# Kernel tuning notes

Measured on AMD Instinct MI355X. Metric: run time of the kernel, lower is better.

## Reference

```python
import jax, jax.numpy as jnp
import numpy as np

N = 50000
IN_F = 128
OUT_F = 128
NRELA = 128
E1 = 400000
E2 = 100000
ALPHA = 0.2   # LeakyReLU slope
D = 0.85      # PageRank damping
EPS = 1e-12


def setup_inputs() -> dict:
    key = jax.random.key(0)
    ks = jax.random.split(key, 8)
    return {
        "input": jax.random.normal(ks[0], (N, IN_F), dtype=jnp.float32),
        "edge": jax.random.randint(ks[1], (2, E1), 0, N, dtype=jnp.int64),
        "edge_embed": jax.random.normal(ks[2], (E1, NRELA), dtype=jnp.float32),
        "edge_list_nhop": jax.random.randint(ks[3], (2, E2), 0, N, dtype=jnp.int64),
        "edge_embed_nhop": jax.random.normal(ks[4], (E2, NRELA), dtype=jnp.float32),
        "entity_rank": jax.random.uniform(ks[5], (N,), dtype=jnp.float32),
        "a": 0.05 * jax.random.normal(ks[6], (OUT_F, 2 * IN_F + NRELA), dtype=jnp.float32),
        "a_2": 0.05 * jax.random.normal(ks[7], (1, OUT_F), dtype=jnp.float32),
    }


def reference(input, edge, edge_embed, edge_list_nhop, edge_embed_nhop, entity_rank, a, a_2):
    n = input.shape[0]
    # concat n-hop edges (len(edge_list_nhop) != 0 path in the original)
    e = jnp.concatenate([edge, edge_list_nhop], axis=1)          # [2, E]
    emb = jnp.concatenate([edge_embed, edge_embed_nhop], axis=0) # [E, nrela]
    src, dst = e[0], e[1]

    # edge MLP: edge_h = [x_src | x_dst | rel]  -> a @ edge_h^T, leakyrelu
    edge_h = jnp.concatenate([input[src], input[dst], emb], axis=1)   # [E, 2*in+nrela]
    edge_m = jax.nn.leaky_relu(edge_h @ a.T, ALPHA)                   # [E, out]
    powers = -jax.nn.leaky_relu(edge_m @ a_2[0], ALPHA)               # [E]
    edge_e = jnp.exp(powers)                                          # [E]

    # softmax-like normalization over incoming edges of each target node
    a_rowsum = jax.ops.segment_sum(edge_e, dst, num_segments=n)       # [N]
    a_rowsum = jnp.where(a_rowsum == 0.0, EPS, a_rowsum)
    rel_att = edge_e / a_rowsum[dst]                                  # [E]

    # PageRank-style rank update
    e_rowsum = jax.ops.segment_sum(rel_att, src, num_segments=n)      # [N] (out-sum)
    e_rowsum = jnp.where(e_rowsum == 0.0, EPS, e_rowsum)
    val = rel_att * entity_rank[src] / e_rowsum[src]                  # [E]
    e_colsum = jax.ops.segment_sum(val, dst, num_segments=n)          # [N]
    new_rank = 1.0 - D + D * e_colsum                                 # [N]

    # rank-weighted attention propagation of edge features
    edge_prop = (rel_att * new_rank[src])[:, None] * edge_m           # [E, out]
    h_prime = jax.ops.segment_sum(edge_prop, dst, num_segments=n)     # [N, out]

    return jax.nn.elu(h_prime), new_rank
```

## Files before the change

kernel.cpp:

```cpp
#include <hip/hip_runtime.h>
#include <math.h>

#define N_NODES 50000
#define E1N 400000
#define E2N 100000
#define E_TOT 500000
#define ALPHAC 0.2f
#define DAMP 0.85f
#define EPSC 1e-12f

typedef __bf16 bf16_t;
typedef __bf16 bf16x8 __attribute__((ext_vector_type(8)));
typedef float f32x16 __attribute__((ext_vector_type(16)));

__device__ __forceinline__ float lrelu(float x) { return x > 0.f ? x : ALPHAC * x; }

__global__ __launch_bounds__(256) void k_pack(const float* __restrict__ a,
                                              bf16_t* __restrict__ bp) {
  int i = blockIdx.x * 256 + threadIdx.x;
  int j = i & 7;
  int l = (i >> 3) & 63;
  int nt = (i >> 9) & 3;
  int ks = i >> 11;
  int k = ks * 16 + ((l >> 5) << 3) + j;
  int o = nt * 32 + (l & 31);
  bp[i] = (bf16_t)a[o * 384 + k];
}

__global__ __launch_bounds__(256) void k_edges(const int* __restrict__ edge,
                                               const int* __restrict__ nhop,
                                               int* __restrict__ sidx,
                                               int* __restrict__ didx, int stride) {
  int e = blockIdx.x * 256 + threadIdx.x;
  if (e >= E_TOT) return;
  if (e < E1N) {
    sidx[e] = edge[(size_t)e * stride];
    didx[e] = edge[(size_t)(E1N + e) * stride];
  } else {
    int t = e - E1N;
    sidx[e] = nhop[(size_t)t * stride];
    didx[e] = nhop[(size_t)(E2N + t) * stride];
  }
}

template <bool ACCUM>
__global__ __launch_bounds__(256, 3) void k_gemm(
    const float* __restrict__ input, const float* __restrict__ eemb,
    const float* __restrict__ eembn, const int* __restrict__ sidx,
    const int* __restrict__ didx, const bf16_t* __restrict__ bpack,
    const float* __restrict__ a2, float* __restrict__ edge_e,
    float* __restrict__ a_rowsum, const float* __restrict__ rel_att,
    const float* __restrict__ new_rank, float* __restrict__ hout) {
  const int tid = threadIdx.x;
  const int lane = tid & 63;
  const int wv = tid >> 6;
  const long long e0w = (long long)blockIdx.x * 128 + wv * 32;
  if (e0w >= E_TOT) return;
  const int m = lane & 31;
  const int hi2 = lane >> 5;
  const long long e = e0w + m;
  const int s = sidx[e];
  const int d = didx[e];
  const float* b0 = input + (size_t)s * 128;
  const float* b1 = input + (size_t)d * 128;
  const float* b2 = (e < E1N) ? (eemb + (size_t)e * 128)
                              : (eembn + (size_t)(e - E1N) * 128);
  const int koff = hi2 << 3;

  const bf16x8* __restrict__ bp = (const bf16x8*)bpack;

  f32x16 acc[4];
#pragma unroll
  for (int nt = 0; nt < 4; ++nt)
#pragma unroll
    for (int r = 0; r < 16; ++r) acc[nt][r] = 0.f;

  auto loadA = [&](int ks) -> bf16x8 {
    const float* p = (ks < 8 ? b0 : (ks < 16 ? b1 : b2)) + ((ks & 7) << 4) + koff;
    float4 u0 = *(const float4*)p;
    float4 u1 = *(const float4*)(p + 4);
    bf16x8 r = {(bf16_t)u0.x, (bf16_t)u0.y, (bf16_t)u0.z, (bf16_t)u0.w,
                (bf16_t)u1.x, (bf16_t)u1.y, (bf16_t)u1.z, (bf16_t)u1.w};
    return r;
  };

  bf16x8 a_cur = loadA(0);
  bf16x8 bb[4], bn[4];
#pragma unroll
  for (int nt = 0; nt < 4; ++nt) bb[nt] = bp[nt * 64 + lane];

#pragma unroll
  for (int ks = 0; ks < 24; ++ks) {
    bf16x8 a_nxt;
    if (ks < 23) {
      a_nxt = loadA(ks + 1);
#pragma unroll
      for (int nt = 0; nt < 4; ++nt) bn[nt] = bp[((ks + 1) * 4 + nt) * 64 + lane];
    }
#pragma unroll
    for (int nt = 0; nt < 4; ++nt)
      acc[nt] = __builtin_amdgcn_mfma_f32_32x32x16_bf16(a_cur, bb[nt], acc[nt], 0, 0, 0);
    a_cur = a_nxt;
#pragma unroll
    for (int nt = 0; nt < 4; ++nt) bb[nt] = bn[nt];
  }

  if (!ACCUM) {
    float sacc[16];
#pragma unroll
    for (int r = 0; r < 16; ++r) sacc[r] = 0.f;
#pragma unroll
    for (int nt = 0; nt < 4; ++nt) {
      float a2v = a2[nt * 32 + m];
#pragma unroll
      for (int r = 0; r < 16; ++r) sacc[r] += lrelu(acc[nt][r]) * a2v;
    }
#pragma unroll
    for (int off = 1; off < 32; off <<= 1) {
#pragma unroll
      for (int r = 0; r < 16; ++r) sacc[r] += __shfl_xor(sacc[r], off, 64);
    }
    if (m == 0) {
#pragma unroll
      for (int r = 0; r < 16; ++r) {
        int row = (r & 3) + ((r >> 2) << 3) + (hi2 << 2);
        long long ee_i = e0w + row;
        float ev = expf(-lrelu(sacc[r]));
        edge_e[ee_i] = ev;
        atomicAdd(&a_rowsum[didx[ee_i]], ev);
      }
    }
  } else {
    float w_m = rel_att[e] * new_rank[s];
    float wr[16];
    int dr[16];
#pragma unroll
    for (int r = 0; r < 16; ++r) {
      int row = (r & 3) + ((r >> 2) << 3) + (hi2 << 2);
      wr[r] = __shfl(w_m, row, 64);
      dr[r] = __shfl(d, row, 64);
    }
#pragma unroll
    for (int nt = 0; nt < 4; ++nt) {
      int o = nt * 32 + m;
#pragma unroll
      for (int r = 0; r < 16; ++r)
        atomicAdd(&hout[(size_t)dr[r] * 128 + o], lrelu(acc[nt][r]) * wr[r]);
    }
  }
}

__global__ __launch_bounds__(256) void k_relatt(const float* __restrict__ edge_e,
                                                const int* __restrict__ didx,
                                                const int* __restrict__ sidx,
                                                const float* __restrict__ a_rowsum,
                                                float* __restrict__ rel_att,
                                                float* __restrict__ e_rowsum) {
  int e = blockIdx.x * 256 + threadIdx.x;
  if (e >= E_TOT) return;
  float rs = a_rowsum[didx[e]];
  rs = (rs == 0.f) ? EPSC : rs;
  float r = edge_e[e] / rs;
  rel_att[e] = r;
  atomicAdd(&e_rowsum[sidx[e]], r);
}

__global__ __launch_bounds__(256) void k_val(const float* __restrict__ rel_att,
                                             const int* __restrict__ sidx,
                                             const int* __restrict__ didx,
                                             const float* __restrict__ rank,
                                             const float* __restrict__ e_rowsum,
                                             float* __restrict__ e_colsum) {
  int e = blockIdx.x * 256 + threadIdx.x;
  if (e >= E_TOT) return;
  int s = sidx[e];
  float er = e_rowsum[s];
  er = (er == 0.f) ? EPSC : er;
  float val = rel_att[e] * rank[s] / er;
  atomicAdd(&e_colsum[didx[e]], val);
}

__global__ __launch_bounds__(256) void k_rank(const float* __restrict__ e_colsum,
                                              float* __restrict__ new_rank,
                                              float* __restrict__ out_tail) {
  int n = blockIdx.x * 256 + threadIdx.x;
  if (n >= N_NODES) return;
  float nr = 1.f - DAMP + DAMP * e_colsum[n];
  new_rank[n] = nr;
  out_tail[n] = nr;
}

__global__ __launch_bounds__(256) void k_elu(float* __restrict__ h) {
  int i = blockIdx.x * 256 + threadIdx.x;
  if (i < N_NODES * 128) {
    float x = h[i];
    h[i] = x > 0.f ? x : expm1f(x);
  }
}

extern "C" void kernel_launch(void* const* d_in, const int* in_sizes, int n_in,
                              void* d_out, int out_size, void* d_ws, size_t ws_size,
                              hipStream_t stream) {
  const float* input = (const float*)d_in[0];
  const int* edge = (const int*)d_in[1];
  const float* eemb = (const float*)d_in[2];
  const int* enh = (const int*)d_in[3];
  const float* eembn = (const float*)d_in[4];
  const float* rank = (const float*)d_in[5];
  const float* a = (const float*)d_in[6];
  const float* a2 = (const float*)d_in[7];
  float* out = (float*)d_out;

  int estride = (in_sizes[1] == 2 * E1N) ? 1 : 2;

  char* ws = (char*)d_ws;
  bf16_t* bpack = (bf16_t*)(ws);
  int* sidx = (int*)(ws + 98304);
  int* didx = (int*)(ws + 2098304);
  float* edge_e = (float*)(ws + 4098304);
  float* rel_att = (float*)(ws + 6098304);
  float* a_rowsum = (float*)(ws + 8098304);
  float* e_rowsum = (float*)(ws + 8298304);
  float* e_colsum = (float*)(ws + 8498304);
  float* new_rank = (float*)(ws + 8698304);

  hipMemsetAsync(a_rowsum, 0, 3 * 200000, stream);
  hipMemsetAsync(out, 0, (size_t)N_NODES * 128 * 4, stream);

  k_pack<<<192, 256, 0, stream>>>(a, bpack);
  k_edges<<<(E_TOT + 255) / 256, 256, 0, stream>>>(edge, enh, sidx, didx, estride);

  const int NB = (E_TOT + 127) / 128;
  const int EB = (E_TOT + 255) / 256;
  k_gemm<false><<<NB, 256, 0, stream>>>(input, eemb, eembn, sidx, didx, bpack, a2,
                                        edge_e, a_rowsum, nullptr, nullptr, nullptr);
  k_relatt<<<EB, 256, 0, stream>>>(edge_e, didx, sidx, a_rowsum, rel_att, e_rowsum);
  k_val<<<EB, 256, 0, stream>>>(rel_att, sidx, didx, rank, e_rowsum, e_colsum);
  k_rank<<<(N_NODES + 255) / 256, 256, 0, stream>>>(e_colsum, new_rank,
                                                    out + (size_t)N_NODES * 128);
  k_gemm<true><<<NB, 256, 0, stream>>>(input, eemb, eembn, sidx, didx, bpack, a2,
                                       nullptr, nullptr, rel_att, new_rank, out);
  k_elu<<<(N_NODES * 128 + 255) / 256, 256, 0, stream>>>(out);
}
```

Baseline: 845.2 us.

## Precompute per-node projections of source and destination features, gather them per edge

```diff
diff --git a/kernel.cpp b/kernel.cpp
--- a/kernel.cpp
+++ b/kernel.cpp
@@ -10,21 +10,38 @@
 #define EPSC 1e-12f
 
 typedef __bf16 bf16_t;
+typedef __bf16 bf16x4 __attribute__((ext_vector_type(4)));
 typedef __bf16 bf16x8 __attribute__((ext_vector_type(8)));
 typedef float f32x16 __attribute__((ext_vector_type(16)));
 
 __device__ __forceinline__ float lrelu(float x) { return x > 0.f ? x : ALPHAC * x; }
 
-__global__ __launch_bounds__(256) void k_pack(const float* __restrict__ a,
-                                              bf16_t* __restrict__ bp) {
+__global__ __launch_bounds__(256) void k_pack12(const float* __restrict__ a,
+                                                bf16_t* __restrict__ bp) {
   int i = blockIdx.x * 256 + threadIdx.x;
+  if (i >= 32768) return;
+  int j = i & 7;
+  int l = (i >> 3) & 63;
+  int nt = (i >> 9) & 7;
+  int ks = i >> 12;
+  int c = nt * 32 + (l & 31);
+  int o = (c < 128) ? c : c - 128;
+  int koff = (c < 128) ? 0 : 128;
+  int k = ks * 16 + ((l >> 5) << 3) + j;
+  bp[i] = (bf16_t)a[o * 384 + koff + k];
+}
+
+__global__ __launch_bounds__(256) void k_pack3(const float* __restrict__ a,
+                                               bf16_t* __restrict__ bp) {
+  int i = blockIdx.x * 256 + threadIdx.x;
+  if (i >= 16384) return;
   int j = i & 7;
   int l = (i >> 3) & 63;
   int nt = (i >> 9) & 3;
   int ks = i >> 11;
+  int o = nt * 32 + (l & 31);
   int k = ks * 16 + ((l >> 5) << 3) + j;
-  int o = nt * 32 + (l & 31);
-  bp[i] = (bf16_t)a[o * 384 + k];
+  bp[i] = (bf16_t)a[o * 384 + 256 + k];
 }
 
 __global__ __launch_bounds__(256) void k_edges(const int* __restrict__ edge,
@@ -43,32 +60,90 @@
   }
 }
 
+__global__ __launch_bounds__(256) void k_uv(const float* __restrict__ input,
+                                            const bf16_t* __restrict__ bp12,
+                                            bf16_t* __restrict__ uv) {
+  const int tid = threadIdx.x, lane = tid & 63, wv = tid >> 6;
+  const int n0 = blockIdx.x * 128 + wv * 32;
+  const int m = lane & 31, hi2 = lane >> 5;
+  int n = n0 + m;
+  if (n >= N_NODES) n = 0;
+  const float* ar = input + (size_t)n * 128 + hi2 * 8;
+  const bf16x8* bp = (const bf16x8*)bp12;
+
+  f32x16 acc[8];
+#pragma unroll
+  for (int nt = 0; nt < 8; ++nt)
+#pragma unroll
+    for (int r = 0; r < 16; ++r) acc[nt][r] = 0.f;
+
+#pragma unroll
+  for (int ks = 0; ks < 8; ++ks) {
+    float4 u0 = *(const float4*)(ar + ks * 16);
+    float4 u1 = *(const float4*)(ar + ks * 16 + 4);
+    bf16x8 af = {(bf16_t)u0.x, (bf16_t)u0.y, (bf16_t)u0.z, (bf16_t)u0.w,
+                 (bf16_t)u1.x, (bf16_t)u1.y, (bf16_t)u1.z, (bf16_t)u1.w};
+#pragma unroll
+    for (int nt = 0; nt < 8; ++nt)
+      acc[nt] = __builtin_amdgcn_mfma_f32_32x32x16_bf16(af, bp[(ks * 8 + nt) * 64 + lane],
+                                                        acc[nt], 0, 0, 0);
+  }
+#pragma unroll
+  for (int nt = 0; nt < 8; ++nt)
+#pragma unroll
+    for (int r = 0; r < 16; ++r) {
+      int row = (r & 3) + ((r >> 2) << 3) + (hi2 << 2);
+      int node = n0 + row;
+      if (node < N_NODES) uv[(size_t)node * 256 + nt * 32 + m] = (bf16_t)acc[nt][r];
+    }
+}
+
 template <bool ACCUM>
-__global__ __launch_bounds__(256, 3) void k_gemm(
-    const float* __restrict__ input, const float* __restrict__ eemb,
-    const float* __restrict__ eembn, const int* __restrict__ sidx,
-    const int* __restrict__ didx, const bf16_t* __restrict__ bpack,
+__global__ __launch_bounds__(256, 3) void k_pass(
+    const float* __restrict__ eemb, const float* __restrict__ eembn,
+    const bf16_t* __restrict__ uv, const int* __restrict__ sidx,
+    const int* __restrict__ didx, const bf16_t* __restrict__ bp3,
     const float* __restrict__ a2, float* __restrict__ edge_e,
     float* __restrict__ a_rowsum, const float* __restrict__ rel_att,
     const float* __restrict__ new_rank, float* __restrict__ hout) {
+  __shared__ bf16_t s_sum[128][136];
   const int tid = threadIdx.x;
+  const long long e0 = (long long)blockIdx.x * 128;
+
+  {
+    const int g = tid >> 5;
+    const int cl = (tid & 31) * 4;
+#pragma unroll
+    for (int i = 0; i < 16; ++i) {
+      int el = i * 8 + g;
+      long long e = e0 + el;
+      float sx = 0.f, sy = 0.f, sz = 0.f, sw = 0.f;
+      if (e < E_TOT) {
+        int s = sidx[e], d = didx[e];
+        bf16x4 u = *(const bf16x4*)(uv + (size_t)s * 256 + cl);
+        bf16x4 v = *(const bf16x4*)(uv + (size_t)d * 256 + 128 + cl);
+        sx = (float)u[0] + (float)v[0];
+        sy = (float)u[1] + (float)v[1];
+        sz = (float)u[2] + (float)v[2];
+        sw = (float)u[3] + (float)v[3];
+      }
+      bf16x4 o = {(bf16_t)sx, (bf16_t)sy, (bf16_t)sz, (bf16_t)sw};
+      *(bf16x4*)&s_sum[el][cl] = o;
+    }
+  }
+  __syncthreads();
+
   const int lane = tid & 63;
   const int wv = tid >> 6;
-  const long long e0w = (long long)blockIdx.x * 128 + wv * 32;
+  const long long e0w = e0 + wv * 32;
   if (e0w >= E_TOT) return;
-  const int m = lane & 31;
-  const int hi2 = lane >> 5;
+  const int m = lane & 31, hi2 = lane >> 5;
   const long long e = e0w + m;
-  const int s = sidx[e];
-  const int d = didx[e];
-  const float* b0 = input + (size_t)s * 128;
-  const float* b1 = input + (size_t)d * 128;
   const float* b2 = (e < E1N) ? (eemb + (size_t)e * 128)
                               : (eembn + (size_t)(e - E1N) * 128);
-  const int koff = hi2 << 3;
-
-  const bf16x8* __restrict__ bp = (const bf16x8*)bpack;
-
+  const float* ar = b2 + hi2 * 8;
+
+  const bf16x8* bp = (const bf16x8*)bp3;
   f32x16 acc[4];
 #pragma unroll
   for (int nt = 0; nt < 4; ++nt)
@@ -76,12 +151,11 @@
     for (int r = 0; r < 16; ++r) acc[nt][r] = 0.f;
 
   auto loadA = [&](int ks) -> bf16x8 {
-    const float* p = (ks < 8 ? b0 : (ks < 16 ? b1 : b2)) + ((ks & 7) << 4) + koff;
-    float4 u0 = *(const float4*)p;
-    float4 u1 = *(const float4*)(p + 4);
-    bf16x8 r = {(bf16_t)u0.x, (bf16_t)u0.y, (bf16_t)u0.z, (bf16_t)u0.w,
-                (bf16_t)u1.x, (bf16_t)u1.y, (bf16_t)u1.z, (bf16_t)u1.w};
-    return r;
+    float4 u0 = *(const float4*)(ar + ks * 16);
+    float4 u1 = *(const float4*)(ar + ks * 16 + 4);
+    bf16x8 rr = {(bf16_t)u0.x, (bf16_t)u0.y, (bf16_t)u0.z, (bf16_t)u0.w,
+                 (bf16_t)u1.x, (bf16_t)u1.y, (bf16_t)u1.z, (bf16_t)u1.w};
+    return rr;
   };
 
   bf16x8 a_cur = loadA(0);
@@ -90,9 +164,9 @@
   for (int nt = 0; nt < 4; ++nt) bb[nt] = bp[nt * 64 + lane];
 
 #pragma unroll
-  for (int ks = 0; ks < 24; ++ks) {
+  for (int ks = 0; ks < 8; ++ks) {
     bf16x8 a_nxt;
-    if (ks < 23) {
+    if (ks < 7) {
       a_nxt = loadA(ks + 1);
 #pragma unroll
       for (int nt = 0; nt < 4; ++nt) bn[nt] = bp[((ks + 1) * 4 + nt) * 64 + lane];
@@ -106,32 +180,38 @@
   }
 
   if (!ACCUM) {
-    float sacc[16];
-#pragma unroll
-    for (int r = 0; r < 16; ++r) sacc[r] = 0.f;
+    float sac[16];
+#pragma unroll
+    for (int r = 0; r < 16; ++r) sac[r] = 0.f;
 #pragma unroll
     for (int nt = 0; nt < 4; ++nt) {
       float a2v = a2[nt * 32 + m];
-#pragma unroll
-      for (int r = 0; r < 16; ++r) sacc[r] += lrelu(acc[nt][r]) * a2v;
+      int o = nt * 32 + m;
+#pragma unroll
+      for (int r = 0; r < 16; ++r) {
+        int row = (r & 3) + ((r >> 2) << 3) + (hi2 << 2);
+        float c = acc[nt][r] + (float)s_sum[wv * 32 + row][o];
+        sac[r] += lrelu(c) * a2v;
+      }
     }
 #pragma unroll
     for (int off = 1; off < 32; off <<= 1) {
 #pragma unroll
-      for (int r = 0; r < 16; ++r) sacc[r] += __shfl_xor(sacc[r], off, 64);
+      for (int r = 0; r < 16; ++r) sac[r] += __shfl_xor(sac[r], off, 64);
     }
     if (m == 0) {
 #pragma unroll
       for (int r = 0; r < 16; ++r) {
         int row = (r & 3) + ((r >> 2) << 3) + (hi2 << 2);
         long long ee_i = e0w + row;
-        float ev = expf(-lrelu(sacc[r]));
+        float ev = expf(-lrelu(sac[r]));
         edge_e[ee_i] = ev;
         atomicAdd(&a_rowsum[didx[ee_i]], ev);
       }
     }
   } else {
-    float w_m = rel_att[e] * new_rank[s];
+    float w_m = rel_att[e] * new_rank[sidx[e]];
+    int d = didx[e];
     float wr[16];
     int dr[16];
 #pragma unroll
@@ -144,8 +224,11 @@
     for (int nt = 0; nt < 4; ++nt) {
       int o = nt * 32 + m;
 #pragma unroll
-      for (int r = 0; r < 16; ++r)
-        atomicAdd(&hout[(size_t)dr[r] * 128 + o], lrelu(acc[nt][r]) * wr[r]);
+      for (int r = 0; r < 16; ++r) {
+        int row = (r & 3) + ((r >> 2) << 3) + (hi2 << 2);
+        float c = acc[nt][r] + (float)s_sum[wv * 32 + row][o];
+        atomicAdd(&hout[(size_t)dr[r] * 128 + o], lrelu(c) * wr[r]);
+      }
     }
   }
 }
@@ -214,31 +297,35 @@
   int estride = (in_sizes[1] == 2 * E1N) ? 1 : 2;
 
   char* ws = (char*)d_ws;
-  bf16_t* bpack = (bf16_t*)(ws);
-  int* sidx = (int*)(ws + 98304);
-  int* didx = (int*)(ws + 2098304);
-  float* edge_e = (float*)(ws + 4098304);
-  float* rel_att = (float*)(ws + 6098304);
-  float* a_rowsum = (float*)(ws + 8098304);
-  float* e_rowsum = (float*)(ws + 8298304);
-  float* e_colsum = (float*)(ws + 8498304);
-  float* new_rank = (float*)(ws + 8698304);
+  bf16_t* bp12 = (bf16_t*)(ws);
+  bf16_t* bp3 = (bf16_t*)(ws + 65536);
+  bf16_t* uv = (bf16_t*)(ws + 98304);
+  int* sidx = (int*)(ws + 25698304);
+  int* didx = (int*)(ws + 27698304);
+  float* edge_e = (float*)(ws + 29698304);
+  float* rel_att = (float*)(ws + 31698304);
+  float* a_rowsum = (float*)(ws + 33698304);
+  float* e_rowsum = (float*)(ws + 33898304);
+  float* e_colsum = (float*)(ws + 34098304);
+  float* new_rank = (float*)(ws + 34298304);
 
   hipMemsetAsync(a_rowsum, 0, 3 * 200000, stream);
   hipMemsetAsync(out, 0, (size_t)N_NODES * 128 * 4, stream);
 
-  k_pack<<<192, 256, 0, stream>>>(a, bpack);
+  k_pack12<<<128, 256, 0, stream>>>(a, bp12);
+  k_pack3<<<64, 256, 0, stream>>>(a, bp3);
   k_edges<<<(E_TOT + 255) / 256, 256, 0, stream>>>(edge, enh, sidx, didx, estride);
+  k_uv<<<(N_NODES + 127) / 128, 256, 0, stream>>>(input, bp12, uv);
 
   const int NB = (E_TOT + 127) / 128;
   const int EB = (E_TOT + 255) / 256;
-  k_gemm<false><<<NB, 256, 0, stream>>>(input, eemb, eembn, sidx, didx, bpack, a2,
+  k_pass<false><<<NB, 256, 0, stream>>>(eemb, eembn, uv, sidx, didx, bp3, a2,
                                         edge_e, a_rowsum, nullptr, nullptr, nullptr);
   k_relatt<<<EB, 256, 0, stream>>>(edge_e, didx, sidx, a_rowsum, rel_att, e_rowsum);
   k_val<<<EB, 256, 0, stream>>>(rel_att, sidx, didx, rank, e_rowsum, e_colsum);
   k_rank<<<(N_NODES + 255) / 256, 256, 0, stream>>>(e_colsum, new_rank,
                                                     out + (size_t)N_NODES * 128);
-  k_gemm<true><<<NB, 256, 0, stream>>>(input, eemb, eembn, sidx, didx, bpack, a2,
+  k_pass<true><<<NB, 256, 0, stream>>>(eemb, eembn, uv, sidx, didx, bp3, a2,
                                        nullptr, nullptr, rel_att, new_rank, out);
   k_elu<<<(N_NODES * 128 + 255) / 256, 256, 0, stream>>>(out);
 }
```

After: 789.4 us. 6.6% less time.
